# Optimization experiments

Hardware: AMD Instinct MI355X
Metric: run time of the kernel (lower is better)

## Reference

```python
import jax, jax.numpy as jnp
import numpy as np
import math

D_MODEL = 1024
N_HEADS = 16
D_K = D_MODEL // N_HEADS  # 64
D_V = D_K


def setup_inputs() -> dict:
    key = jax.random.key(0)
    ks = jax.random.split(key, 11)
    B, S = 64, 2048
    s = 1.0 / math.sqrt(D_MODEL)
    so = 1.0 / math.sqrt(N_HEADS * D_V)
    return {
        "q": jax.random.normal(ks[0], (B, 1, D_MODEL), jnp.float32),
        "k": jax.random.normal(ks[1], (B, S, D_MODEL), jnp.float32),
        "v": jax.random.normal(ks[2], (B, S, D_MODEL), jnp.float32),
        "Wq": jax.random.normal(ks[3], (D_MODEL, N_HEADS * D_K), jnp.float32) * s,
        "bq": jnp.zeros((N_HEADS * D_K,), jnp.float32),
        "Wk": jax.random.normal(ks[4], (D_MODEL, N_HEADS * D_K), jnp.float32) * s,
        "bk": jnp.zeros((N_HEADS * D_K,), jnp.float32),
        "Wv": jax.random.normal(ks[5], (D_MODEL, N_HEADS * D_V), jnp.float32) * s,
        "bv": jnp.zeros((N_HEADS * D_V,), jnp.float32),
        "Wo": jax.random.normal(ks[6], (N_HEADS * D_V, D_MODEL), jnp.float32) * so,
        "bo": jnp.zeros((D_MODEL,), jnp.float32),
    }


def reference(q, k, v, Wq, bq, Wk, bk, Wv, bv, Wo, bo):
    B = q.shape[0]
    # single-linear Q/K/V projections (MLP with 2-entry dim_list has no activation)
    qh = (q @ Wq + bq).reshape(B, -1, N_HEADS, D_K).transpose(0, 2, 1, 3)  # [B,H,1,dk]
    kh = (k @ Wk + bk).reshape(B, -1, N_HEADS, D_K).transpose(0, 2, 1, 3)  # [B,H,S,dk]
    vh = (v @ Wv + bv).reshape(B, -1, N_HEADS, D_V).transpose(0, 2, 1, 3)  # [B,H,S,dv]
    scores = jnp.einsum("bhqd,bhkd->bhqk", qh, kh) / math.sqrt(D_K)
    attn = jax.nn.softmax(scores, axis=-1)  # dropout is identity in eval mode
    out = jnp.einsum("bhqk,bhkd->bhqd", attn, vh)  # [B,H,1,dv]
    concat = out.transpose(0, 2, 1, 3).reshape(B, N_HEADS * D_V)  # requires q_len==1
    # out MLP with last_act=True -> ReLU after linear
    return jax.nn.relu(concat @ Wo + bo)
```

## Files before the change

### kernel.cpp

```cpp
#include <hip/hip_runtime.h>
#include <math.h>

#define D_MODEL 1024
#define N_HEADS 16
#define D_K 64
#define B_SZ 64
#define S_LEN 2048

__global__ __launch_bounds__(256) void k_qproj(const float* __restrict__ q,
                                               const float* __restrict__ Wq,
                                               const float* __restrict__ bq,
                                               const float* __restrict__ Wk,
                                               float* __restrict__ qt) {
    int b = blockIdx.x >> 4, h = blockIdx.x & 15;
    int t = threadIdx.x;
    __shared__ float ql[D_MODEL];
    __shared__ float qsl[D_K];
    __shared__ float4 red[256];
    ((float4*)ql)[t] = ((const float4*)(q + (size_t)b * D_MODEL))[t];
    __syncthreads();
    int j4 = t & 15, dg = t >> 4;
    float4 a = make_float4(0.f, 0.f, 0.f, 0.f);
#pragma unroll 8
    for (int i = 0; i < 64; ++i) {
        int d = i * 16 + dg;
        float4 w4 = *(const float4*)(Wq + (size_t)d * D_MODEL + h * D_K + 4 * j4);
        float s = ql[d];
        a.x = fmaf(s, w4.x, a.x);
        a.y = fmaf(s, w4.y, a.y);
        a.z = fmaf(s, w4.z, a.z);
        a.w = fmaf(s, w4.w, a.w);
    }
    red[t] = a;
    __syncthreads();
    if (t < 16) {
        float4 r = make_float4(0.f, 0.f, 0.f, 0.f);
#pragma unroll
        for (int g = 0; g < 16; ++g) {
            float4 x = red[g * 16 + t];
            r.x += x.x; r.y += x.y; r.z += x.z; r.w += x.w;
        }
        float4 bb = *(const float4*)(bq + h * D_K + 4 * t);
        r.x += bb.x; r.y += bb.y; r.z += bb.z; r.w += bb.w;
        *(float4*)(qsl + 4 * t) = r;
    }
    __syncthreads();
#pragma unroll
    for (int p = 0; p < 4; ++p) {
        int d = p * 256 + t;
        const float* w = Wk + (size_t)d * D_MODEL + h * D_K;
        float acc = 0.f;
#pragma unroll
        for (int j4i = 0; j4i < 16; ++j4i) {
            float4 w4 = ((const float4*)w)[j4i];
            float4 q4 = ((const float4*)qsl)[j4i];
            acc += w4.x * q4.x + w4.y * q4.y + w4.z * q4.z + w4.w * q4.w;
        }
        qt[((size_t)(b * N_HEADS + h)) * D_MODEL + d] = acc * 0.125f;
    }
}

#define ST 256
#define DC 32
#define KROW 36
__global__ __launch_bounds__(256) void k_attn(const float* __restrict__ k,
                                              const float* __restrict__ v,
                                              const float* __restrict__ qt,
                                              float* __restrict__ part,
                                              float* __restrict__ ml) {
    __shared__ float kt[ST * KROW];
    __shared__ float qtl[N_HEADS * DC];
    __shared__ float al[N_HEADS * 256];
    int b = blockIdx.x >> 3;
    int ch = blockIdx.x & 7;
    int t = threadIdx.x;
    int w = t >> 6, lane = t & 63;
    int s0 = ch * ST;
    const float* kbase = k + ((size_t)b * S_LEN + s0) * D_MODEL;
    const float* qtbase = qt + (size_t)b * N_HEADS * D_MODEL;
    float acc[4][4] = {};
    for (int dc = 0; dc < D_MODEL; dc += DC) {
#pragma unroll
        for (int p = 0; p < 8; ++p) {
            int idx = t + 256 * p;
            int s = idx >> 3, d4 = idx & 7;
            float4 v4 = *(const float4*)(kbase + (size_t)s * D_MODEL + dc + 4 * d4);
            *(float4*)(kt + s * KROW + 4 * d4) = v4;
        }
        if (t < 128) {
            int hh = t >> 3, d4 = t & 7;
            *(float4*)(qtl + hh * DC + 4 * d4) =
                *(const float4*)(qtbase + (size_t)hh * D_MODEL + dc + 4 * d4);
        }
        __syncthreads();
#pragma unroll
        for (int d4 = 0; d4 < DC / 4; ++d4) {
            float4 qv[4], kv[4];
#pragma unroll
            for (int j = 0; j < 4; ++j) qv[j] = *(const float4*)(qtl + (4 * w + j) * DC + 4 * d4);
#pragma unroll
            for (int i = 0; i < 4; ++i) kv[i] = *(const float4*)(kt + (64 * i + lane) * KROW + 4 * d4);
#pragma unroll
            for (int i = 0; i < 4; ++i)
#pragma unroll
                for (int j = 0; j < 4; ++j)
                    acc[i][j] = fmaf(kv[i].x, qv[j].x,
                                fmaf(kv[i].y, qv[j].y,
                                fmaf(kv[i].z, qv[j].z,
                                fmaf(kv[i].w, qv[j].w, acc[i][j]))));
        }
        __syncthreads();
    }
#pragma unroll
    for (int j = 0; j < 4; ++j) {
        float mx = fmaxf(fmaxf(acc[0][j], acc[1][j]), fmaxf(acc[2][j], acc[3][j]));
#pragma unroll
        for (int o = 32; o; o >>= 1) mx = fmaxf(mx, __shfl_xor(mx, o, 64));
        float p0 = __expf(acc[0][j] - mx);
        float p1 = __expf(acc[1][j] - mx);
        float p2 = __expf(acc[2][j] - mx);
        float p3 = __expf(acc[3][j] - mx);
        float l = p0 + p1 + p2 + p3;
#pragma unroll
        for (int o = 32; o; o >>= 1) l += __shfl_xor(l, o, 64);
        int h = 4 * w + j;
        al[h * 256 + lane] = p0;
        al[h * 256 + 64 + lane] = p1;
        al[h * 256 + 128 + lane] = p2;
        al[h * 256 + 192 + lane] = p3;
        if (lane == 0) {
            size_t mi = (((size_t)ch * B_SZ + b) * N_HEADS + h) * 2;
            ml[mi] = mx;
            ml[mi + 1] = l;
        }
    }
    __syncthreads();
    float4 acc4[N_HEADS];
#pragma unroll
    for (int h = 0; h < N_HEADS; ++h) acc4[h] = make_float4(0.f, 0.f, 0.f, 0.f);
    const float* vbase = v + ((size_t)b * S_LEN + s0) * D_MODEL + 4 * t;
    for (int sg = 0; sg < 64; ++sg) {
        float4 v0 = *(const float4*)(vbase + (size_t)(4 * sg + 0) * D_MODEL);
        float4 v1 = *(const float4*)(vbase + (size_t)(4 * sg + 1) * D_MODEL);
        float4 v2 = *(const float4*)(vbase + (size_t)(4 * sg + 2) * D_MODEL);
        float4 v3 = *(const float4*)(vbase + (size_t)(4 * sg + 3) * D_MODEL);
#pragma unroll
        for (int h = 0; h < N_HEADS; ++h) {
            float4 a4 = *(const float4*)(al + h * 256 + 4 * sg);
            acc4[h].x = fmaf(a4.x, v0.x, fmaf(a4.y, v1.x, fmaf(a4.z, v2.x, fmaf(a4.w, v3.x, acc4[h].x))));
            acc4[h].y = fmaf(a4.x, v0.y, fmaf(a4.y, v1.y, fmaf(a4.z, v2.y, fmaf(a4.w, v3.y, acc4[h].y))));
            acc4[h].z = fmaf(a4.x, v0.z, fmaf(a4.y, v1.z, fmaf(a4.z, v2.z, fmaf(a4.w, v3.z, acc4[h].z))));
            acc4[h].w = fmaf(a4.x, v0.w, fmaf(a4.y, v1.w, fmaf(a4.z, v2.w, fmaf(a4.w, v3.w, acc4[h].w))));
        }
    }
#pragma unroll
    for (int h = 0; h < N_HEADS; ++h)
        *(float4*)(part + (((size_t)ch * B_SZ + b) * N_HEADS + h) * D_MODEL + 4 * t) = acc4[h];
}

__global__ __launch_bounds__(256) void k_cc(const float* __restrict__ part,
                                            const float* __restrict__ ml,
                                            const float* __restrict__ Wv,
                                            const float* __restrict__ bv,
                                            float* __restrict__ cc) {
    int b = blockIdx.x >> 4, h = blockIdx.x & 15;
    int t = threadIdx.x;
    __shared__ float vt[D_MODEL];
    __shared__ float4 red[256];
    float m8[8], l8[8];
#pragma unroll
    for (int ch = 0; ch < 8; ++ch) {
        size_t mi = (((size_t)ch * B_SZ + b) * N_HEADS + h) * 2;
        m8[ch] = ml[mi];
        l8[ch] = ml[mi + 1];
    }
    float M = m8[0];
#pragma unroll
    for (int ch = 1; ch < 8; ++ch) M = fmaxf(M, m8[ch]);
    float wgt[8];
    float L = 0.f;
#pragma unroll
    for (int ch = 0; ch < 8; ++ch) {
        wgt[ch] = __expf(m8[ch] - M);
        L = fmaf(l8[ch], wgt[ch], L);
    }
    float invL = 1.0f / L;
    float4 s = make_float4(0.f, 0.f, 0.f, 0.f);
#pragma unroll
    for (int ch = 0; ch < 8; ++ch) {
        float4 x = *(const float4*)(part + (((size_t)ch * B_SZ + b) * N_HEADS + h) * D_MODEL + 4 * t);
        s.x = fmaf(wgt[ch], x.x, s.x);
        s.y = fmaf(wgt[ch], x.y, s.y);
        s.z = fmaf(wgt[ch], x.z, s.z);
        s.w = fmaf(wgt[ch], x.w, s.w);
    }
    s.x *= invL; s.y *= invL; s.z *= invL; s.w *= invL;
    *(float4*)(vt + 4 * t) = s;
    __syncthreads();
    int j4 = t & 15, dg = t >> 4;
    float4 a = make_float4(0.f, 0.f, 0.f, 0.f);
#pragma unroll 8
    for (int i = 0; i < 64; ++i) {
        int d = i * 16 + dg;
        float4 w4 = *(const float4*)(Wv + (size_t)d * D_MODEL + h * D_K + 4 * j4);
        float sv = vt[d];
        a.x = fmaf(sv, w4.x, a.x);
        a.y = fmaf(sv, w4.y, a.y);
        a.z = fmaf(sv, w4.z, a.z);
        a.w = fmaf(sv, w4.w, a.w);
    }
    red[t] = a;
    __syncthreads();
    if (t < 16) {
        float4 r = make_float4(0.f, 0.f, 0.f, 0.f);
#pragma unroll
        for (int g = 0; g < 16; ++g) {
            float4 x = red[g * 16 + t];
            r.x += x.x; r.y += x.y; r.z += x.z; r.w += x.w;
        }
        float4 bb = *(const float4*)(bv + h * D_K + 4 * t);
        r.x += bb.x; r.y += bb.y; r.z += bb.z; r.w += bb.w;
        *(float4*)(cc + (size_t)b * D_MODEL + h * D_K + 4 * t) = r;
    }
}

__global__ __launch_bounds__(256) void k_out(const float* __restrict__ cc,
                                             const float* __restrict__ Wo,
                                             const float* __restrict__ bo,
                                             float* __restrict__ out) {
    int b = blockIdx.x >> 2, nc = blockIdx.x & 3;
    int t = threadIdx.x;
    __shared__ float cl[D_MODEL];
    __shared__ float4 red[256];
    ((float4*)cl)[t] = ((const float4*)(cc + (size_t)b * D_MODEL))[t];
    __syncthreads();
    int n4 = t & 63, dg = t >> 6;
    float4 a = make_float4(0.f, 0.f, 0.f, 0.f);
#pragma unroll 8
    for (int i = 0; i < 256; ++i) {
        int d = dg * 256 + i;
        float4 w4 = *(const float4*)(Wo + (size_t)d * D_MODEL + nc * 256 + 4 * n4);
        float s = cl[d];
        a.x = fmaf(s, w4.x, a.x);
        a.y = fmaf(s, w4.y, a.y);
        a.z = fmaf(s, w4.z, a.z);
        a.w = fmaf(s, w4.w, a.w);
    }
    red[t] = a;
    __syncthreads();
    if (t < 64) {
        float4 r = red[t];
#pragma unroll
        for (int g = 1; g < 4; ++g) {
            float4 x = red[g * 64 + t];
            r.x += x.x; r.y += x.y; r.z += x.z; r.w += x.w;
        }
        float4 bb = *(const float4*)(bo + nc * 256 + 4 * t);
        r.x += bb.x; r.y += bb.y; r.z += bb.z; r.w += bb.w;
        r.x = r.x > 0.f ? r.x : 0.f;
        r.y = r.y > 0.f ? r.y : 0.f;
        r.z = r.z > 0.f ? r.z : 0.f;
        r.w = r.w > 0.f ? r.w : 0.f;
        *(float4*)(out + (size_t)b * D_MODEL + nc * 256 + 4 * t) = r;
    }
}

extern "C" void kernel_launch(void* const* d_in, const int* in_sizes, int n_in,
                              void* d_out, int out_size, void* d_ws, size_t ws_size,
                              hipStream_t stream) {
    const float* q  = (const float*)d_in[0];
    const float* k  = (const float*)d_in[1];
    const float* v  = (const float*)d_in[2];
    const float* Wq = (const float*)d_in[3];
    const float* bq = (const float*)d_in[4];
    const float* Wk = (const float*)d_in[5];
    const float* Wv = (const float*)d_in[7];
    const float* bv = (const float*)d_in[8];
    const float* Wo = (const float*)d_in[9];
    const float* bo = (const float*)d_in[10];
    float* out = (float*)d_out;

    float* ws = (float*)d_ws;
    float* qt   = ws;
    float* part = qt + 1048576;
    float* ml   = part + 8388608;
    float* cc   = ml + 16384;

    k_qproj<<<1024, 256, 0, stream>>>(q, Wq, bq, Wk, qt);
    k_attn<<<512, 256, 0, stream>>>(k, v, qt, part, ml);
    k_cc<<<1024, 256, 0, stream>>>(part, ml, Wv, bv, cc);
    k_out<<<256, 256, 0, stream>>>(cc, Wo, bo, out);
}
```

Measured before the change: 330.7 us.

## Double-buffer K tiles via direct global-to-LDS loads with XOR swizzle

The score loop in the attention kernel now loads K chunks straight into LDS with global_load_lds, double-buffering both the K tile and the projected-q tile so the next chunk's fetch overlaps the current chunk's FMA work. The padded KROW layout gives way to an XOR-swizzled layout to avoid bank conflicts, and the softmax scratch buffer aliases the K buffer to keep LDS usage in check. The change trades simpler code for hand-placed waitcnt and barrier calls, which could race or stall if the counts are wrong.

```diff
diff --git a/kernel.cpp b/kernel.cpp
--- a/kernel.cpp
+++ b/kernel.cpp
@@ -60,17 +60,22 @@
     }
 }
 
+__device__ __forceinline__ void gload16(const float* g, float* l) {
+    __builtin_amdgcn_global_load_lds((const __attribute__((address_space(1))) void*)g,
+                                     (__attribute__((address_space(3))) void*)l, 16, 0, 0);
+}
+
 #define ST 256
 #define DC 32
-#define KROW 36
+#define KTF (ST * DC)
 __global__ __launch_bounds__(256) void k_attn(const float* __restrict__ k,
                                               const float* __restrict__ v,
                                               const float* __restrict__ qt,
                                               float* __restrict__ part,
                                               float* __restrict__ ml) {
-    __shared__ float kt[ST * KROW];
-    __shared__ float qtl[N_HEADS * DC];
-    __shared__ float al[N_HEADS * 256];
+    __shared__ float kt2[2 * KTF];
+    __shared__ float qt2[2 * N_HEADS * DC];
+    float* al = kt2;
     int b = blockIdx.x >> 3;
     int ch = blockIdx.x & 7;
     int t = threadIdx.x;
@@ -78,28 +83,48 @@
     int s0 = ch * ST;
     const float* kbase = k + ((size_t)b * S_LEN + s0) * D_MODEL;
     const float* qtbase = qt + (size_t)b * N_HEADS * D_MODEL;
+    int lr = lane >> 3, lc = lane & 7;
+    int csw = 4 * (lc ^ lr);
+    int lsw4 = 4 * (lane & 7);
+    int qh_ = t >> 4, qc2 = 2 * (t & 15);
+
+    float2 qcur = *(const float2*)(qtbase + (size_t)qh_ * D_MODEL + qc2);
+#pragma unroll
+    for (int p = 0; p < 8; ++p) {
+        int s_i = w * 8 + p;
+        gload16(kbase + (size_t)(s_i * 8 + lr) * D_MODEL + csw, kt2 + s_i * 256);
+    }
+    asm volatile("s_waitcnt vmcnt(0)" ::: "memory");
+    *(float2*)(qt2 + qh_ * DC + qc2) = qcur;
+    asm volatile("s_waitcnt lgkmcnt(0)" ::: "memory");
+    __builtin_amdgcn_s_barrier();
+    __builtin_amdgcn_sched_barrier(0);
+
     float acc[4][4] = {};
-    for (int dc = 0; dc < D_MODEL; dc += DC) {
-#pragma unroll
-        for (int p = 0; p < 8; ++p) {
-            int idx = t + 256 * p;
-            int s = idx >> 3, d4 = idx & 7;
-            float4 v4 = *(const float4*)(kbase + (size_t)s * D_MODEL + dc + 4 * d4);
-            *(float4*)(kt + s * KROW + 4 * d4) = v4;
-        }
-        if (t < 128) {
-            int hh = t >> 3, d4 = t & 7;
-            *(float4*)(qtl + hh * DC + 4 * d4) =
-                *(const float4*)(qtbase + (size_t)hh * D_MODEL + dc + 4 * d4);
-        }
-        __syncthreads();
+    for (int it = 0; it < 32; ++it) {
+        int buf = it & 1;
+        float2 qnext = make_float2(0.f, 0.f);
+        if (it < 31) {
+            int dcn = (it + 1) * DC;
+            qnext = *(const float2*)(qtbase + (size_t)qh_ * D_MODEL + dcn + qc2);
+#pragma unroll
+            for (int p = 0; p < 8; ++p) {
+                int s_i = w * 8 + p;
+                gload16(kbase + (size_t)(s_i * 8 + lr) * D_MODEL + dcn + csw,
+                        kt2 + (buf ^ 1) * KTF + s_i * 256);
+            }
+        }
+        __builtin_amdgcn_sched_barrier(0);
+        const float* ktb = kt2 + buf * KTF;
+        const float* qtb = qt2 + buf * (N_HEADS * DC);
 #pragma unroll
         for (int d4 = 0; d4 < DC / 4; ++d4) {
             float4 qv[4], kv[4];
 #pragma unroll
-            for (int j = 0; j < 4; ++j) qv[j] = *(const float4*)(qtl + (4 * w + j) * DC + 4 * d4);
-#pragma unroll
-            for (int i = 0; i < 4; ++i) kv[i] = *(const float4*)(kt + (64 * i + lane) * KROW + 4 * d4);
+            for (int j = 0; j < 4; ++j) qv[j] = *(const float4*)(qtb + (4 * w + j) * DC + 4 * d4);
+#pragma unroll
+            for (int i = 0; i < 4; ++i)
+                kv[i] = *(const float4*)(ktb + (64 * i + lane) * DC + ((4 * d4) ^ lsw4));
 #pragma unroll
             for (int i = 0; i < 4; ++i)
 #pragma unroll
@@ -109,7 +134,13 @@
                                 fmaf(kv[i].z, qv[j].z,
                                 fmaf(kv[i].w, qv[j].w, acc[i][j]))));
         }
-        __syncthreads();
+        if (it < 31) {
+            asm volatile("s_waitcnt vmcnt(0)" ::: "memory");
+            *(float2*)(qt2 + (buf ^ 1) * (N_HEADS * DC) + qh_ * DC + qc2) = qnext;
+        }
+        asm volatile("s_waitcnt lgkmcnt(0)" ::: "memory");
+        __builtin_amdgcn_s_barrier();
+        __builtin_amdgcn_sched_barrier(0);
     }
 #pragma unroll
     for (int j = 0; j < 4; ++j) {
```

Result: slower. 398.6 us (+20.5%).
